# Kernel optimization log

Measured on AMD Instinct MI355X. Metric: run time of the kernel, lower is better.

The kernel has to match this reference:

```python
import jax, jax.numpy as jnp
import numpy as np

NEG_SLOPE = 0.01  # torch leaky_relu default
EPS = 1e-12      # torch F.normalize default


def _edge_mlp(edge_attr, w1, b1, w2, b2, d_h):
    # Sequential(Linear, ReLU, Linear) -> per-edge weight matrices [E, d_h, d_h]
    h = jax.nn.relu(edge_attr @ w1 + b1)
    return (h @ w2 + b2).reshape(-1, d_h, d_h)


def _nnconv(h, src, dst, w_edge, root, bias, n_nodes):
    # message_j->i = x_j @ Theta(e_ji); aggregate (add) at dst; add root transform + bias
    msg = jnp.einsum('ei,eio->eo', h[src], w_edge)  # [E, d_h]
    agg = jax.ops.segment_sum(msg, dst, num_segments=n_nodes)
    return agg + h @ root + bias


def setup_inputs() -> dict:
    key = jax.random.key(0)
    ks = jax.random.split(key, 20)
    N, E, G = 20000, 200000, 128
    d_node, d_edge, d_h, d_out = 64, 16, 32, 32

    x = jax.random.normal(ks[0], (N, d_node), dtype=jnp.float32)
    edge_index = jax.random.randint(ks[1], (2, E), 0, N, dtype=jnp.int32)
    edge_attr = jax.random.normal(ks[2], (E, d_edge), dtype=jnp.float32)
    batch = jnp.sort(jax.random.randint(ks[3], (N,), 0, G, dtype=jnp.int32))

    def lin(k, fan_in, fan_out):
        kw, kb = jax.random.split(k)
        s = 1.0 / np.sqrt(fan_in)
        w = jax.random.uniform(kw, (fan_in, fan_out), jnp.float32, -s, s)
        b = jax.random.uniform(kb, (fan_out,), jnp.float32, -s, s)
        return w, b

    nfc_w, nfc_b = lin(ks[4], d_node, d_h)
    efc1_w1, efc1_b1 = lin(ks[5], d_edge, d_h)
    efc1_w2, efc1_b2 = lin(ks[6], d_h, d_h * d_h)
    root1 = jax.random.uniform(ks[7], (d_h, d_h), jnp.float32, -1/np.sqrt(d_h), 1/np.sqrt(d_h))
    bias1 = jnp.zeros((d_h,), jnp.float32)
    efc2_w1, efc2_b1 = lin(ks[8], d_edge, d_h)
    efc2_w2, efc2_b2 = lin(ks[9], d_h, d_h * d_h)
    root2 = jax.random.uniform(ks[10], (d_h, d_h), jnp.float32, -1/np.sqrt(d_h), 1/np.sqrt(d_h))
    bias2 = jnp.zeros((d_h,), jnp.float32)
    fc_w, fc_b = lin(ks[11], d_h, d_out)

    return dict(x=x, edge_index=edge_index, edge_attr=edge_attr, batch=batch,
                num_graphs=G,
                nfc_w=nfc_w, nfc_b=nfc_b,
                efc1_w1=efc1_w1, efc1_b1=efc1_b1, efc1_w2=efc1_w2, efc1_b2=efc1_b2,
                root1=root1, bias1=bias1,
                efc2_w1=efc2_w1, efc2_b1=efc2_b1, efc2_w2=efc2_w2, efc2_b2=efc2_b2,
                root2=root2, bias2=bias2,
                fc_w=fc_w, fc_b=fc_b)


def reference(x, edge_index, edge_attr, batch, num_graphs,
              nfc_w, nfc_b,
              efc1_w1, efc1_b1, efc1_w2, efc1_b2, root1, bias1,
              efc2_w1, efc2_b1, efc2_w2, efc2_b2, root2, bias2,
              fc_w, fc_b):
    n_nodes = x.shape[0]
    d_h = nfc_w.shape[1]
    src, dst = edge_index[0], edge_index[1]

    lrelu = lambda v: jax.nn.leaky_relu(v, NEG_SLOPE)
    # dropout(p=0.1) is identity at inference
    h = lrelu(x @ nfc_w + nfc_b)

    w_e1 = _edge_mlp(edge_attr, efc1_w1, efc1_b1, efc1_w2, efc1_b2, d_h)
    h = lrelu(_nnconv(h, src, dst, w_e1, root1, bias1, n_nodes))

    w_e2 = _edge_mlp(edge_attr, efc2_w1, efc2_b1, efc2_w2, efc2_b2, d_h)
    atom_embs = lrelu(_nnconv(h, src, dst, w_e2, root2, bias2, n_nodes))

    pooled = jax.ops.segment_sum(atom_embs, batch, num_segments=num_graphs)  # [G, d_h]
    norm = jnp.linalg.norm(pooled, ord=2, axis=1, keepdims=True)
    pooled = pooled / jnp.maximum(norm, EPS)

    out = pooled @ fc_w + fc_b
    return (out, atom_embs)
```

## Files before the change

kernel.cpp:

```cpp
#include <hip/hip_runtime.h>
#include <stdint.h>

#define NN 20000
#define NE 200000
#define NG 128
#define NWJOBS 3125
#define EBLK 256

typedef __attribute__((ext_vector_type(8))) short short8;
typedef __attribute__((ext_vector_type(4))) float f32x4;
typedef __attribute__((ext_vector_type(4))) int   int4v;
typedef __attribute__((ext_vector_type(2))) unsigned int uint2v;

static __device__ __forceinline__ float bf2f(short s) {
    union { unsigned int u; float f; } x;
    x.u = ((unsigned int)(unsigned short)s) << 16;
    return x.f;
}
static __device__ __forceinline__ unsigned short f2bf(float f) {
    unsigned int u = __builtin_bit_cast(unsigned int, f);
    u += 0x7fffu + ((u >> 16) & 1u);
    return (unsigned short)(u >> 16);
}
static __device__ __forceinline__ unsigned int pack2bf(float a, float b) {
    unsigned int u0 = __builtin_bit_cast(unsigned int, a) + 0x8000u;
    unsigned int u1 = __builtin_bit_cast(unsigned int, b) + 0x8000u;
    return __builtin_amdgcn_perm(u1, u0, 0x07060302u);
}
static __device__ __forceinline__ int detect_isbf(const unsigned int* x) {
    unsigned int u = x[threadIdx.x & 63];
    unsigned int el = (u >> 7) & 0xffu;
    unsigned long long bm = __ballot((el >= 100u) && (el <= 140u));
    return __popcll(bm) > 32;
}

__global__ __launch_bounds__(256) void k_prep_all(
    const void* x, const void* nfcw, const void* nfcb,
    const void* root1, const void* bias1,
    const void* w2a, const void* b2a, const void* w2b, const void* b2b,
    const void* w1a, const void* b1a, const void* w1b, const void* b1b,
    const void* ea,
    float* __restrict__ h0, float* __restrict__ aggA, float* __restrict__ aggB,
    short* __restrict__ W2Ta, short* __restrict__ W2Tb,
    short* __restrict__ w1t_ws, float* __restrict__ b1f_ws,
    short* __restrict__ ea_ws) {
    const int isbf = detect_isbf((const unsigned int*)x);
    const int b = blockIdx.x;

    if (b < 2500) {
        __shared__ float wf[64 * 32];
        __shared__ float rf[32 * 32];
        __shared__ float bfs[32];
        __shared__ float rb[32];
        __shared__ float xrow[8][66];
        __shared__ float hrow[8][33];
        for (int i = threadIdx.x; i < 64 * 32; i += 256)
            wf[i] = isbf ? bf2f(((const short*)nfcw)[i]) : ((const float*)nfcw)[i];
        for (int i = threadIdx.x; i < 32 * 32; i += 256)
            rf[i] = isbf ? bf2f(((const short*)root1)[i]) : ((const float*)root1)[i];
        if (threadIdx.x < 32) {
            bfs[threadIdx.x] = isbf ? bf2f(((const short*)nfcb)[threadIdx.x])
                                    : ((const float*)nfcb)[threadIdx.x];
            rb[threadIdx.x]  = isbf ? bf2f(((const short*)bias1)[threadIdx.x])
                                    : ((const float*)bias1)[threadIdx.x];
        }
        int t = b * 256 + threadIdx.x;
        int v = t >> 5, c = t & 31, vl = threadIdx.x >> 5;
        if (isbf) {
            const short* xr = (const short*)x + (size_t)v * 64;
            xrow[vl][c]      = bf2f(xr[c]);
            xrow[vl][32 + c] = bf2f(xr[32 + c]);
        } else {
            const float* xr = (const float*)x + (size_t)v * 64;
            xrow[vl][c]      = xr[c];
            xrow[vl][32 + c] = xr[32 + c];
        }
        __syncthreads();
        float acc = bfs[c];
#pragma unroll
        for (int q = 0; q < 64; ++q) acc += xrow[vl][q] * wf[q * 32 + c];
        float hv = acc > 0.f ? acc : 0.01f * acc;
        h0[t] = hv;
        hrow[vl][c] = hv;
        __syncthreads();
        float a2 = rb[c];
#pragma unroll
        for (int q = 0; q < 32; ++q) a2 += hrow[vl][q] * rf[q * 32 + c];
        aggA[t] = a2;
        return;
    }
    if (b < 4327) {
        const int bb = b - 2500;
        if (bb == 1) {
            for (int i = threadIdx.x; i < 1024; i += 256) {
                int layer = i >> 9, jj = i & 511, c = jj >> 4, q = jj & 15;
                const void* w1p = layer ? w1b : w1a;
                w1t_ws[i] = isbf ? ((const short*)w1p)[q * 32 + c]
                                 : (short)f2bf(((const float*)w1p)[q * 32 + c]);
            }
            for (int i = threadIdx.x; i < 64; i += 256) {
                int layer = i >> 5, c = i & 31;
                const void* b1p = layer ? b1b : b1a;
                b1f_ws[i] = isbf ? bf2f(((const short*)b1p)[c])
                                 : ((const float*)b1p)[c];
            }
        }
        int t = bb * 256 + threadIdx.x;
        if (t < 2 * 32 * 1056) {
            int layer = t / (32 * 1056);
            int r = t - layer * (32 * 1056);
            int o = r / 1056, kp = r - o * 1056;
            const void* w2 = layer ? w2b : w2a;
            const void* b2 = layer ? b2b : b2a;
            int idx; const void* sp;
            if (kp < 1024) { int kk = kp >> 5, i = kp & 31; idx = kk * 1024 + i * 32 + o; sp = w2; }
            else           { int i = kp - 1024;             idx = i * 32 + o;             sp = b2; }
            short v = isbf ? ((const short*)sp)[idx] : (short)f2bf(((const float*)sp)[idx]);
            (layer ? W2Tb : W2Ta)[o * 1056 + kp] = v;
            return;
        }
        int u = t - 2 * 32 * 1056;
        if (u < NE * 2 && !isbf) {
            const float* p = (const float*)ea + (size_t)u * 8;
            f32x4 f0 = *(const f32x4*)p;
            f32x4 f1 = *(const f32x4*)(p + 4);
            union { unsigned int d[4]; short8 v; } o8;
            o8.d[0] = pack2bf(f0[0], f0[1]);
            o8.d[1] = pack2bf(f0[2], f0[3]);
            o8.d[2] = pack2bf(f1[0], f1[1]);
            o8.d[3] = pack2bf(f1[2], f1[3]);
            *(short8*)&ea_ws[(size_t)u * 8] = o8.v;
        }
        return;
    }
    {
        int idx = (b - 4327) * 256 + threadIdx.x;
        if (idx < NN * 32 / 4) {
            f32x4 z = {0.f, 0.f, 0.f, 0.f};
            ((f32x4*)aggB)[idx] = z;
        }
    }
}

__global__ __launch_bounds__(1024, 4) void k_edge(
    const float* __restrict__ h_in,
    const short* __restrict__ W2T,
    const short* __restrict__ w1pre,
    const float* __restrict__ b1pre,
    const int* __restrict__ src, const int* __restrict__ dst,
    const short* __restrict__ ea_bf,
    const short* __restrict__ ea_ws,
    const unsigned int* xdet,
    float* agg,
    const int layer2, const void* rootp, const void* biasp) {
    __shared__ __align__(16) short w2t[32 * 1058];
    __shared__ __align__(16) short h1l[16 * 32 * 68];

    const int isbf = detect_isbf(xdet);
    const short* eap = isbf ? ea_bf : ea_ws;

    for (int c = threadIdx.x; c < 32 * 132; c += 1024) {
        int o = c / 132, t8 = c - o * 132;
        *(short8*)&w2t[o * 1058 + (t8 << 3)] = *(const short8*)&W2T[o * 1056 + (t8 << 3)];
    }
    if (layer2) {
        const int base = blockIdx.x * 2500;
        for (int i = threadIdx.x; i < 2500; i += 1024) {
            int t = base + i;
            int v = t >> 5, c = t & 31;
            const float* ar = h_in + (size_t)v * 32;
            float acc = isbf ? bf2f(((const short*)biasp)[c]) : ((const float*)biasp)[c];
#pragma unroll
            for (int q = 0; q < 32; ++q) {
                float hv = ar[q];
                hv = hv > 0.f ? hv : 0.01f * hv;
                float wv = isbf ? bf2f(((const short*)rootp)[q * 32 + c])
                                : ((const float*)rootp)[q * 32 + c];
                acc += hv * wv;
            }
            atomicAdd(&agg[t], acc);
        }
    }
    __syncthreads();

    const int lane = threadIdx.x & 63;
    const int wid  = threadIdx.x >> 6;
    const int m    = lane & 15;
    const int quad = lane >> 4;
    const int wb   = wid * (32 * 68);

    const int w = wid * EBLK + (int)blockIdx.x;
    if (w >= NWJOBS) return;

    short8 w1lo = {0, 0, 0, 0, 0, 0, 0, 0};
    short8 w1hi = {0, 0, 0, 0, 0, 0, 0, 0};
    if (quad < 2) {
        w1lo = *(const short8*)&w1pre[m * 16 + ((quad & 1) << 3)];
        w1hi = *(const short8*)&w1pre[(m + 16) * 16 + ((quad & 1) << 3)];
    }
    const float b1lo = b1pre[m];
    const float b1hi = b1pre[m + 16];
    const f32x4 zero4 = {0.f, 0.f, 0.f, 0.f};

    const int e0 = w << 6;
    short8 eafc[4];
    f32x4 hs[4][2];
    int4v dv[4];
    {
        int s0[4];
#pragma unroll
        for (int mt = 0; mt < 4; ++mt) {
            eafc[mt] = *(const short8*)&eap[(size_t)(e0 + mt * 16 + m) * 16 + ((quad & 1) << 3)];
            s0[mt] = src[e0 + mt * 16 + m];
            dv[mt] = *(const int4v*)&dst[e0 + mt * 16 + (quad << 2)];
        }
#pragma unroll
        for (int mt = 0; mt < 4; ++mt) {
            const float* hr = h_in + (size_t)s0[mt] * 32 + (quad << 3);
            hs[mt][0] = *(const f32x4*)hr;
            hs[mt][1] = *(const f32x4*)(hr + 4);
        }
    }

#pragma unroll
    for (int mt = 0; mt < 4; ++mt) {
        f32x4 alo = __builtin_amdgcn_mfma_f32_16x16x32_bf16(eafc[mt], w1lo, zero4, 0, 0, 0);
        f32x4 ahi = __builtin_amdgcn_mfma_f32_16x16x32_bf16(eafc[mt], w1hi, zero4, 0, 0, 0);
        float v0 = fmaxf(alo[0] + b1lo, 0.f);
        float v1 = fmaxf(alo[1] + b1lo, 0.f);
        float v2 = fmaxf(alo[2] + b1lo, 0.f);
        float v3 = fmaxf(alo[3] + b1lo, 0.f);
        uint2v dlo; dlo[0] = pack2bf(v0, v1); dlo[1] = pack2bf(v2, v3);
        *(uint2v*)&h1l[wb + m * 68 + (mt << 4) + (quad << 2)] = dlo;
        v0 = fmaxf(ahi[0] + b1hi, 0.f);
        v1 = fmaxf(ahi[1] + b1hi, 0.f);
        v2 = fmaxf(ahi[2] + b1hi, 0.f);
        v3 = fmaxf(ahi[3] + b1hi, 0.f);
        uint2v dhi; dhi[0] = pack2bf(v0, v1); dhi[1] = pack2bf(v2, v3);
        *(uint2v*)&h1l[wb + (m + 16) * 68 + (mt << 4) + (quad << 2)] = dhi;
    }
    __asm volatile("s_waitcnt lgkmcnt(0)" ::: "memory");

    short8 hsbf[4];
#pragma unroll
    for (int mt = 0; mt < 4; ++mt) {
        f32x4 g0 = hs[mt][0], g1 = hs[mt][1];
        if (layer2) {
#pragma unroll
            for (int p = 0; p < 4; ++p) {
                g0[p] = g0[p] > 0.f ? g0[p] : 0.01f * g0[p];
                g1[p] = g1[p] > 0.f ? g1[p] : 0.01f * g1[p];
            }
        }
        union { unsigned int du[4]; short8 v; } a;
        a.du[0] = pack2bf(g0[0], g0[1]);
        a.du[1] = pack2bf(g0[2], g0[3]);
        a.du[2] = pack2bf(g1[0], g1[1]);
        a.du[3] = pack2bf(g1[2], g1[3]);
        hsbf[mt] = a.v;
    }

    f32x4 acc0[4] = {zero4, zero4, zero4, zero4};
    f32x4 acc1[4] = {zero4, zero4, zero4, zero4};
#pragma unroll
    for (int s = 0; s < 33; ++s) {
        short8 bf0 = *(const short8*)&w2t[m * 1058 + (s << 5) + (quad << 3)];
        short8 bf1 = *(const short8*)&w2t[(m + 16) * 1058 + (s << 5) + (quad << 3)];
        if (s < 32) {
#pragma unroll
            for (int mt = 0; mt < 4; ++mt) {
                uint2v hd = *(const uint2v*)&h1l[wb + s * 68 + (mt << 4) + (quad << 2)];
                f32x4 hv;
                hv[0] = __builtin_bit_cast(float, hd[0] << 16);
                hv[1] = __builtin_bit_cast(float, hd[0] & 0xffff0000u);
                hv[2] = __builtin_bit_cast(float, hd[1] << 16);
                hv[3] = __builtin_bit_cast(float, hd[1] & 0xffff0000u);
                f32x4 u0 = __builtin_amdgcn_mfma_f32_16x16x32_bf16(hsbf[mt], bf0, zero4, 0, 0, 0);
                f32x4 u1 = __builtin_amdgcn_mfma_f32_16x16x32_bf16(hsbf[mt], bf1, zero4, 0, 0, 0);
                acc0[mt] += hv * u0;
                acc1[mt] += hv * u1;
            }
        } else {
#pragma unroll
            for (int mt = 0; mt < 4; ++mt) {
                acc0[mt] = __builtin_amdgcn_mfma_f32_16x16x32_bf16(hsbf[mt], bf0, acc0[mt], 0, 0, 0);
                acc1[mt] = __builtin_amdgcn_mfma_f32_16x16x32_bf16(hsbf[mt], bf1, acc1[mt], 0, 0, 0);
            }
        }
    }

#pragma unroll
    for (int mt = 0; mt < 4; ++mt) {
#pragma unroll
        for (int r = 0; r < 4; ++r) {
            float* ap = agg + (size_t)dv[mt][r] * 32 + m;
            atomicAdd(ap, acc0[mt][r]);
            atomicAdd(ap + 16, acc1[mt][r]);
        }
    }
}

__global__ __launch_bounds__(256) void k_final(
    const float* __restrict__ agg, const int* __restrict__ batch,
    const unsigned int* xdet, void* __restrict__ out,
    const void* fcw, const void* fcb) {
    const int isbf = detect_isbf(xdet);
    const int g = blockIdx.x;
    __shared__ int srange[2];
    __shared__ float gacc[8][32];
    __shared__ float pn[32];
    if (threadIdx.x < 2) {
        int target = g + (int)threadIdx.x;
        int lo = 0, hi = NN;
        while (lo < hi) {
            int mid = (lo + hi) >> 1;
            if (batch[mid] < target) lo = mid + 1; else hi = mid;
        }
        srange[threadIdx.x] = lo;
    }
    __syncthreads();
    const int ns = srange[0], ne = srange[1];
    const int c = threadIdx.x & 31;
    float psum = 0.f;
    for (int idx = ns * 32 + threadIdx.x; idx < ne * 32; idx += 256) {
        float v = agg[idx];
        v = v > 0.f ? v : 0.01f * v;
        if (isbf) ((short*)out)[4096 + idx] = (short)f2bf(v);
        else      ((float*)out)[4096 + idx] = v;
        psum += v;
    }
    gacc[threadIdx.x >> 5][c] = psum;
    __syncthreads();
    if (threadIdx.x < 32) {
        float p = 0.f;
#pragma unroll
        for (int r = 0; r < 8; ++r) p += gacc[r][threadIdx.x];
        float sq = p * p;
#pragma unroll
        for (int o = 16; o > 0; o >>= 1) sq += __shfl_xor(sq, o, 64);
        float inv = 1.0f / fmaxf(sqrtf(sq), 1e-12f);
        pn[threadIdx.x] = p * inv;
    }
    __syncthreads();
    if (threadIdx.x < 32) {
        const int t = threadIdx.x;
        float acc = isbf ? bf2f(((const short*)fcb)[t]) : ((const float*)fcb)[t];
#pragma unroll
        for (int q = 0; q < 32; ++q) {
            float wv = isbf ? bf2f(((const short*)fcw)[q * 32 + t])
                            : ((const float*)fcw)[q * 32 + t];
            acc += pn[q] * wv;
        }
        if (isbf) ((short*)out)[g * 32 + t] = (short)f2bf(acc);
        else      ((float*)out)[g * 32 + t] = acc;
    }
}

extern "C" void kernel_launch(void* const* d_in, const int* in_sizes, int n_in,
                              void* d_out, int out_size, void* d_ws, size_t ws_size,
                              hipStream_t stream) {
    (void)in_sizes; (void)n_in; (void)out_size; (void)ws_size;
    const void* x     = d_in[0];
    const int*  eidx  = (const int*)d_in[1];
    const void* ea    = d_in[2];
    const int*  batch = (const int*)d_in[3];
    const void* nfcw  = d_in[5];
    const void* nfcb  = d_in[6];
    const void* e1w1  = d_in[7];
    const void* e1b1  = d_in[8];
    const void* e1w2  = d_in[9];
    const void* e1b2  = d_in[10];
    const void* root1 = d_in[11];
    const void* bias1 = d_in[12];
    const void* e2w1  = d_in[13];
    const void* e2b1  = d_in[14];
    const void* e2w2  = d_in[15];
    const void* e2b2  = d_in[16];
    const void* root2 = d_in[17];
    const void* bias2 = d_in[18];
    const void* fcw   = d_in[19];
    const void* fcb   = d_in[20];
    const unsigned int* xdet = (const unsigned int*)x;

    char* ws = (char*)d_ws;
    float* h0     = (float*)ws; ws += (size_t)NN * 32 * 4;
    float* aggA   = (float*)ws; ws += (size_t)NN * 32 * 4;
    float* aggB   = (float*)ws; ws += (size_t)NN * 32 * 4;
    short* W2T1   = (short*)ws; ws += 32 * 1056 * 2;
    short* W2T2   = (short*)ws; ws += 32 * 1056 * 2;
    short* w1t_ws = (short*)ws; ws += 1024 * 2;
    float* b1f_ws = (float*)ws; ws += 64 * 4;
    short* ea_ws  = (short*)ws; ws += (size_t)NE * 16 * 2;

    const int* srcp = eidx;
    const int* dstp = eidx + NE;

    k_prep_all<<<4952, 256, 0, stream>>>(
        x, nfcw, nfcb, root1, bias1,
        e1w2, e1b2, e2w2, e2b2, e1w1, e1b1, e2w1, e2b1, ea,
        h0, aggA, aggB, W2T1, W2T2, w1t_ws, b1f_ws, ea_ws);

    k_edge<<<EBLK, 1024, 0, stream>>>(h0, W2T1, w1t_ws, b1f_ws, srcp, dstp,
                                      (const short*)ea, ea_ws, xdet, aggA,
                                      0, nullptr, nullptr);
    k_edge<<<EBLK, 1024, 0, stream>>>(aggA, W2T2, w1t_ws + 512, b1f_ws + 32, srcp, dstp,
                                      (const short*)ea, ea_ws, xdet, aggB,
                                      1, root2, bias2);
    k_final<<<NG, 256, 0, stream>>>(aggB, batch, xdet, d_out, fcw, fcb);
}
```

Before: 196.2 us.

## Split edge kernel over K-halves with persistent 256-thread blocks and prefetch

Each edge block now handles half of the hidden dimension of the edge-MLP output weights (K split across paired blocks), so only half of W2T is staged in LDS and each block computes only its half of the first-layer hidden units. Blocks become 256 threads in a 1024-block grid, each wave processing 32-edge jobs in a grid-stride loop, with the next job's edge attributes, source features and destinations prefetched during compute. This is meant to cut LDS footprint and raise occupancy while hiding gather latency. In exchange, the x@root term (the 33rd K step) is done only by one half, the source gather happens twice per edge (once per half), and the partial results are combined through atomics at twice the count.

```diff
diff --git a/kernel.cpp b/kernel.cpp
--- a/kernel.cpp
+++ b/kernel.cpp
@@ -4,8 +4,8 @@
 #define NN 20000
 #define NE 200000
 #define NG 128
-#define NWJOBS 3125
-#define EBLK 256
+#define NJOBS 6250
+#define SLOTS 2048
 
 typedef __attribute__((ext_vector_type(8))) short short8;
 typedef __attribute__((ext_vector_type(4))) float f32x4;
@@ -142,7 +142,7 @@
     }
 }
 
-__global__ __launch_bounds__(1024, 4) void k_edge(
+__global__ __launch_bounds__(256, 4) void k_edge(
     const float* __restrict__ h_in,
     const short* __restrict__ W2T,
     const short* __restrict__ w1pre,
@@ -153,19 +153,31 @@
     const unsigned int* xdet,
     float* agg,
     const int layer2, const void* rootp, const void* biasp) {
-    __shared__ __align__(16) short w2t[32 * 1058];
-    __shared__ __align__(16) short h1l[16 * 32 * 68];
+    __shared__ __align__(16) short w2t[32 * 546];
+    __shared__ __align__(16) short h1l[4 * 16 * 36];
 
     const int isbf = detect_isbf(xdet);
     const short* eap = isbf ? ea_bf : ea_ws;
 
-    for (int c = threadIdx.x; c < 32 * 132; c += 1024) {
-        int o = c / 132, t8 = c - o * 132;
-        *(short8*)&w2t[o * 1058 + (t8 << 3)] = *(const short8*)&W2T[o * 1056 + (t8 << 3)];
-    }
+    const int half = blockIdx.x & 1;
+    const int k0   = half ? 512 : 0;
+    const int S17  = half;
+    const int KS   = 546;
+    const int KLEN = half ? 544 : 512;
+
+    {
+        int cpr = KLEN >> 3;
+        int chunks = 32 * cpr;
+        for (int idx = threadIdx.x; idx < chunks; idx += 256) {
+            int o = idx / cpr, t8 = idx - o * cpr;
+            *(short8*)&w2t[o * KS + (t8 << 3)] =
+                *(const short8*)&W2T[o * 1056 + k0 + (t8 << 3)];
+        }
+    }
+
     if (layer2) {
-        const int base = blockIdx.x * 2500;
-        for (int i = threadIdx.x; i < 2500; i += 1024) {
+        const int base = blockIdx.x * 625;
+        for (int i = threadIdx.x; i < 625; i += 256) {
             int t = base + i;
             int v = t >> 5, c = t & 31;
             const float* ar = h_in + (size_t)v * 32;
@@ -187,89 +199,117 @@
     const int wid  = threadIdx.x >> 6;
     const int m    = lane & 15;
     const int quad = lane >> 4;
-    const int wb   = wid * (32 * 68);
-
-    const int w = wid * EBLK + (int)blockIdx.x;
-    if (w >= NWJOBS) return;
-
-    short8 w1lo = {0, 0, 0, 0, 0, 0, 0, 0};
-    short8 w1hi = {0, 0, 0, 0, 0, 0, 0, 0};
+    const int wb   = wid * (16 * 36);
+
+    short8 w1frag = {0, 0, 0, 0, 0, 0, 0, 0};
     if (quad < 2) {
-        w1lo = *(const short8*)&w1pre[m * 16 + ((quad & 1) << 3)];
-        w1hi = *(const short8*)&w1pre[(m + 16) * 16 + ((quad & 1) << 3)];
-    }
-    const float b1lo = b1pre[m];
-    const float b1hi = b1pre[m + 16];
+        int c = m + (half << 4);
+        w1frag = *(const short8*)&w1pre[c * 16 + ((quad & 1) << 3)];
+    }
+    const float b1v = b1pre[m + (half << 4)];
     const f32x4 zero4 = {0.f, 0.f, 0.f, 0.f};
 
-    const int e0 = w << 6;
-    short8 eafc[4];
-    f32x4 hs[4][2];
-    int4v dv[4];
+    int j = (blockIdx.x >> 1) * 4 + wid;
+
+    short8 eafc[2];
+    f32x4 hs[2][2];
+    int srcn[2];
+    int4v dvc[2];
     {
-        int s0[4];
-#pragma unroll
-        for (int mt = 0; mt < 4; ++mt) {
+        const int e0 = j << 5;
+        int s0[2];
+#pragma unroll
+        for (int mt = 0; mt < 2; ++mt) {
             eafc[mt] = *(const short8*)&eap[(size_t)(e0 + mt * 16 + m) * 16 + ((quad & 1) << 3)];
             s0[mt] = src[e0 + mt * 16 + m];
-            dv[mt] = *(const int4v*)&dst[e0 + mt * 16 + (quad << 2)];
-        }
-#pragma unroll
-        for (int mt = 0; mt < 4; ++mt) {
+        }
+#pragma unroll
+        for (int mt = 0; mt < 2; ++mt) {
             const float* hr = h_in + (size_t)s0[mt] * 32 + (quad << 3);
             hs[mt][0] = *(const f32x4*)hr;
             hs[mt][1] = *(const f32x4*)(hr + 4);
         }
-    }
-
-#pragma unroll
-    for (int mt = 0; mt < 4; ++mt) {
-        f32x4 alo = __builtin_amdgcn_mfma_f32_16x16x32_bf16(eafc[mt], w1lo, zero4, 0, 0, 0);
-        f32x4 ahi = __builtin_amdgcn_mfma_f32_16x16x32_bf16(eafc[mt], w1hi, zero4, 0, 0, 0);
-        float v0 = fmaxf(alo[0] + b1lo, 0.f);
-        float v1 = fmaxf(alo[1] + b1lo, 0.f);
-        float v2 = fmaxf(alo[2] + b1lo, 0.f);
-        float v3 = fmaxf(alo[3] + b1lo, 0.f);
-        uint2v dlo; dlo[0] = pack2bf(v0, v1); dlo[1] = pack2bf(v2, v3);
-        *(uint2v*)&h1l[wb + m * 68 + (mt << 4) + (quad << 2)] = dlo;
-        v0 = fmaxf(ahi[0] + b1hi, 0.f);
-        v1 = fmaxf(ahi[1] + b1hi, 0.f);
-        v2 = fmaxf(ahi[2] + b1hi, 0.f);
-        v3 = fmaxf(ahi[3] + b1hi, 0.f);
-        uint2v dhi; dhi[0] = pack2bf(v0, v1); dhi[1] = pack2bf(v2, v3);
-        *(uint2v*)&h1l[wb + (m + 16) * 68 + (mt << 4) + (quad << 2)] = dhi;
-    }
-    __asm volatile("s_waitcnt lgkmcnt(0)" ::: "memory");
-
-    short8 hsbf[4];
-#pragma unroll
-    for (int mt = 0; mt < 4; ++mt) {
-        f32x4 g0 = hs[mt][0], g1 = hs[mt][1];
-        if (layer2) {
-#pragma unroll
-            for (int p = 0; p < 4; ++p) {
-                g0[p] = g0[p] > 0.f ? g0[p] : 0.01f * g0[p];
-                g1[p] = g1[p] > 0.f ? g1[p] : 0.01f * g1[p];
-            }
-        }
-        union { unsigned int du[4]; short8 v; } a;
-        a.du[0] = pack2bf(g0[0], g0[1]);
-        a.du[1] = pack2bf(g0[2], g0[3]);
-        a.du[2] = pack2bf(g1[0], g1[1]);
-        a.du[3] = pack2bf(g1[2], g1[3]);
-        hsbf[mt] = a.v;
-    }
-
-    f32x4 acc0[4] = {zero4, zero4, zero4, zero4};
-    f32x4 acc1[4] = {zero4, zero4, zero4, zero4};
-#pragma unroll
-    for (int s = 0; s < 33; ++s) {
-        short8 bf0 = *(const short8*)&w2t[m * 1058 + (s << 5) + (quad << 3)];
-        short8 bf1 = *(const short8*)&w2t[(m + 16) * 1058 + (s << 5) + (quad << 3)];
-        if (s < 32) {
-#pragma unroll
-            for (int mt = 0; mt < 4; ++mt) {
-                uint2v hd = *(const uint2v*)&h1l[wb + s * 68 + (mt << 4) + (quad << 2)];
+#pragma unroll
+        for (int mt = 0; mt < 2; ++mt)
+            dvc[mt] = *(const int4v*)&dst[e0 + mt * 16 + (quad << 2)];
+        const int en = (j + SLOTS) < NJOBS ? ((j + SLOTS) << 5) : 0;
+#pragma unroll
+        for (int mt = 0; mt < 2; ++mt) srcn[mt] = src[en + mt * 16 + m];
+    }
+
+    while (j < NJOBS) {
+        const int jn = j + SLOTS;
+
+#pragma unroll
+        for (int mt = 0; mt < 2; ++mt) {
+            f32x4 hacc = __builtin_amdgcn_mfma_f32_16x16x32_bf16(
+                eafc[mt], w1frag, zero4, 0, 0, 0);
+            float v0 = fmaxf(hacc[0] + b1v, 0.f);
+            float v1 = fmaxf(hacc[1] + b1v, 0.f);
+            float v2 = fmaxf(hacc[2] + b1v, 0.f);
+            float v3 = fmaxf(hacc[3] + b1v, 0.f);
+            uint2v dl; dl[0] = pack2bf(v0, v1); dl[1] = pack2bf(v2, v3);
+            *(uint2v*)&h1l[wb + m * 36 + (mt << 4) + (quad << 2)] = dl;
+        }
+        __asm volatile("s_waitcnt lgkmcnt(0)" ::: "memory");
+
+        if (jn < NJOBS) {
+            const int en = jn << 5;
+#pragma unroll
+            for (int mt = 0; mt < 2; ++mt)
+                eafc[mt] = *(const short8*)&eap[(size_t)(en + mt * 16 + m) * 16 + ((quad & 1) << 3)];
+        }
+
+        short8 hsbf[2];
+#pragma unroll
+        for (int mt = 0; mt < 2; ++mt) {
+            f32x4 g0 = hs[mt][0], g1 = hs[mt][1];
+            if (layer2) {
+#pragma unroll
+                for (int p = 0; p < 4; ++p) {
+                    g0[p] = g0[p] > 0.f ? g0[p] : 0.01f * g0[p];
+                    g1[p] = g1[p] > 0.f ? g1[p] : 0.01f * g1[p];
+                }
+            }
+            union { unsigned int du[4]; short8 v; } a;
+            a.du[0] = pack2bf(g0[0], g0[1]);
+            a.du[1] = pack2bf(g0[2], g0[3]);
+            a.du[2] = pack2bf(g1[0], g1[1]);
+            a.du[3] = pack2bf(g1[2], g1[3]);
+            hsbf[mt] = a.v;
+        }
+
+        int4v dvn[2] = {dvc[0], dvc[1]};
+        if (jn < NJOBS) {
+#pragma unroll
+            for (int mt = 0; mt < 2; ++mt) {
+                const float* hr = h_in + (size_t)srcn[mt] * 32 + (quad << 3);
+                hs[mt][0] = *(const f32x4*)hr;
+                hs[mt][1] = *(const f32x4*)(hr + 4);
+            }
+            const int en = jn << 5;
+#pragma unroll
+            for (int mt = 0; mt < 2; ++mt)
+                dvn[mt] = *(const int4v*)&dst[en + mt * 16 + (quad << 2)];
+            const int jn2 = jn + SLOTS;
+            if (jn2 < NJOBS) {
+                const int en2 = jn2 << 5;
+#pragma unroll
+                for (int mt = 0; mt < 2; ++mt) srcn[mt] = src[en2 + mt * 16 + m];
+            }
+        }
+
+        f32x4 acc0[2], acc1[2];
+#pragma unroll
+        for (int mt = 0; mt < 2; ++mt) { acc0[mt] = zero4; acc1[mt] = zero4; }
+
+#pragma unroll
+        for (int s = 0; s < 16; ++s) {
+            short8 bf0 = *(const short8*)&w2t[m * KS + (s << 5) + (quad << 3)];
+            short8 bf1 = *(const short8*)&w2t[(m + 16) * KS + (s << 5) + (quad << 3)];
+#pragma unroll
+            for (int mt = 0; mt < 2; ++mt) {
+                uint2v hd = *(const uint2v*)&h1l[wb + s * 36 + (mt << 4) + (quad << 2)];
                 f32x4 hv;
                 hv[0] = __builtin_bit_cast(float, hd[0] << 16);
                 hv[1] = __builtin_bit_cast(float, hd[0] & 0xffff0000u);
@@ -280,23 +320,30 @@
                 acc0[mt] += hv * u0;
                 acc1[mt] += hv * u1;
             }
-        } else {
-#pragma unroll
-            for (int mt = 0; mt < 4; ++mt) {
+        }
+        if (S17) {
+            const int s = 16;
+            short8 bf0 = *(const short8*)&w2t[m * KS + (s << 5) + (quad << 3)];
+            short8 bf1 = *(const short8*)&w2t[(m + 16) * KS + (s << 5) + (quad << 3)];
+#pragma unroll
+            for (int mt = 0; mt < 2; ++mt) {
                 acc0[mt] = __builtin_amdgcn_mfma_f32_16x16x32_bf16(hsbf[mt], bf0, acc0[mt], 0, 0, 0);
                 acc1[mt] = __builtin_amdgcn_mfma_f32_16x16x32_bf16(hsbf[mt], bf1, acc1[mt], 0, 0, 0);
             }
         }
-    }
-
-#pragma unroll
-    for (int mt = 0; mt < 4; ++mt) {
-#pragma unroll
-        for (int r = 0; r < 4; ++r) {
-            float* ap = agg + (size_t)dv[mt][r] * 32 + m;
-            atomicAdd(ap, acc0[mt][r]);
-            atomicAdd(ap + 16, acc1[mt][r]);
-        }
+
+#pragma unroll
+        for (int mt = 0; mt < 2; ++mt) {
+#pragma unroll
+            for (int r = 0; r < 4; ++r) {
+                float* ap = agg + (size_t)dvc[mt][r] * 32 + m;
+                atomicAdd(ap, acc0[mt][r]);
+                atomicAdd(ap + 16, acc1[mt][r]);
+            }
+        }
+        dvc[0] = dvn[0];
+        dvc[1] = dvn[1];
+        j = jn;
     }
 }
 
@@ -400,11 +447,11 @@
         e1w2, e1b2, e2w2, e2b2, e1w1, e1b1, e2w1, e2b1, ea,
         h0, aggA, aggB, W2T1, W2T2, w1t_ws, b1f_ws, ea_ws);
 
-    k_edge<<<EBLK, 1024, 0, stream>>>(h0, W2T1, w1t_ws, b1f_ws, srcp, dstp,
-                                      (const short*)ea, ea_ws, xdet, aggA,
-                                      0, nullptr, nullptr);
-    k_edge<<<EBLK, 1024, 0, stream>>>(aggA, W2T2, w1t_ws + 512, b1f_ws + 32, srcp, dstp,
-                                      (const short*)ea, ea_ws, xdet, aggB,
-                                      1, root2, bias2);
+    k_edge<<<1024, 256, 0, stream>>>(h0, W2T1, w1t_ws, b1f_ws, srcp, dstp,
+                                     (const short*)ea, ea_ws, xdet, aggA,
+                                     0, nullptr, nullptr);
+    k_edge<<<1024, 256, 0, stream>>>(aggA, W2T2, w1t_ws + 512, b1f_ws + 32, srcp, dstp,
+                                     (const short*)ea, ea_ws, xdet, aggB,
+                                     1, root2, bias2);
     k_final<<<NG, 256, 0, stream>>>(aggB, batch, xdet, d_out, fcw, fcb);
 }
```

New measurement: 237.4 us. 1.21x slower.
